# Optimization experiments

Measured on AMD Instinct MI355X. Metric: run time of the kernel, lower is better.

## Reference

```python
import jax, jax.numpy as jnp
import numpy as np

B, S, D, H = 2, 2048, 2048, 16
HD = D // H  # 128


def _rope(t, cos, sin):
    # t: [B, S, H, HD]; cos/sin: [S, HD//2]
    te, to = t[..., ::2], t[..., 1::2]
    c = cos[None, :, None, :]
    s = sin[None, :, None, :]
    re = te * c - to * s
    im = te * s + to * c
    # interleave back (matches tf.stack(..., axis=-1) + reshape)
    return jnp.stack([re, im], axis=-1).reshape(t.shape)


def setup_inputs() -> dict:
    key = jax.random.key(0)
    ks = jax.random.split(key, 6)
    x = jax.random.normal(ks[0], (B, S, D), dtype=jnp.float32)
    Wq = jax.random.normal(ks[1], (D, D), dtype=jnp.float32) * 0.02
    Wk = jax.random.normal(ks[2], (D, D), dtype=jnp.float32) * 0.02
    Wv = jax.random.normal(ks[3], (D, D), dtype=jnp.float32) * 0.02
    Wo = jax.random.normal(ks[4], (D, D), dtype=jnp.float32) * 0.02
    # rotary embeddings: freqs_cis = exp(i * pos * inv_freq)
    inv_freq = 1.0 / (10000.0 ** (jnp.arange(0, HD, 2, dtype=jnp.float32) / HD))  # [HD//2]
    angles = jnp.arange(S, dtype=jnp.float32)[:, None] * inv_freq[None, :]  # [S, HD//2]
    freqs_cos = jnp.cos(angles)
    freqs_sin = jnp.sin(angles)
    # additive causal mask [1,1,S,S]
    causal = jnp.tril(jnp.ones((S, S), dtype=bool))
    mask = jnp.where(causal, 0.0, -1e9).astype(jnp.float32)[None, None]
    return {"x": x, "Wq": Wq, "Wk": Wk, "Wv": Wv, "Wo": Wo,
            "freqs_cos": freqs_cos, "freqs_sin": freqs_sin, "mask": mask}


def reference(x, Wq, Wk, Wv, Wo, freqs_cos, freqs_sin, mask):
    b, s, d = x.shape
    xq = (x @ Wq).reshape(b, s, H, HD)
    xk = (x @ Wk).reshape(b, s, H, HD)
    xv = (x @ Wv).reshape(b, s, H, HD)
    xq = _rope(xq, freqs_cos, freqs_sin)
    xk = _rope(xk, freqs_cos, freqs_sin)
    # [B, H, S, HD]
    xq = xq.transpose(0, 2, 1, 3)
    xk = xk.transpose(0, 2, 1, 3)
    xv = xv.transpose(0, 2, 1, 3)
    scores = jnp.einsum('bhqd,bhkd->bhqk', xq, xk) / jnp.sqrt(jnp.float32(HD))
    scores = scores + mask[:, :, :s, :s]
    probs = jax.nn.softmax(scores + 1e-9, axis=-1)
    out = jnp.einsum('bhqk,bhkd->bhqd', probs, xv)
    out = out.transpose(0, 2, 1, 3).reshape(b, s, d)
    return out @ Wo
```

## Files before the change

### kernel.cpp

```cpp
#include <hip/hip_runtime.h>
#include <cstdint>

#define BB 2
#define SS 2048
#define DD 2048
#define HH 16
#define HDIM 128
#define MM (BB * SS)

typedef __attribute__((ext_vector_type(8))) short bf16x8;
typedef __attribute__((ext_vector_type(4))) short bf16x4;
typedef __attribute__((ext_vector_type(4))) float f32x4;
typedef __attribute__((ext_vector_type(16))) float f32x16;

__device__ inline short f2bf(float f) {
  union { float f; unsigned u; } v; v.f = f;
  unsigned r = v.u + 0x7FFFu + ((v.u >> 16) & 1u);
  return (short)(r >> 16);
}
__device__ inline float bf2f(short s) {
  union { float f; unsigned u; } v;
  v.u = ((unsigned)(unsigned short)s) << 16;
  return v.f;
}
__device__ inline float asf(int u) { union { int i; float f; } v; v.i = u; return v.f; }
__device__ inline int asi(float f) { union { float f; int i; } v; v.f = f; return v.i; }

__device__ inline unsigned cvtpk_bf16(float lo, float hi) {
  unsigned r;
  asm("v_cvt_pk_bf16_f32 %0, %1, %2" : "=v"(r) : "v"(lo), "v"(hi));
  return r;
}

__device__ inline void gll16(const void* g, void* l) {
  __builtin_amdgcn_global_load_lds(
      (const __attribute__((address_space(1))) void*)g,
      (__attribute__((address_space(3))) void*)l, 16, 0, 0);
}

__global__ __launch_bounds__(256) void cast_bf16_kernel(
    const float* __restrict__ x, short* __restrict__ y, int n4) {
  int i = blockIdx.x * 256 + threadIdx.x;
  if (i >= n4) return;
  float4 v = reinterpret_cast<const float4*>(x)[i];
  bf16x4 o;
  o[0] = f2bf(v.x); o[1] = f2bf(v.y); o[2] = f2bf(v.z); o[3] = f2bf(v.w);
  reinterpret_cast<bf16x4*>(y)[i] = o;
}

__global__ __launch_bounds__(256) void transpose_cast_kernel(
    const float* __restrict__ W, short* __restrict__ Wt) {
  __shared__ short tile[64][65];
  int c = threadIdx.x & 63, r4 = threadIdx.x >> 6;
  int n0 = blockIdx.x << 6, k0 = blockIdx.y << 6;
#pragma unroll
  for (int p = 0; p < 16; ++p) {
    int r = (p << 2) + r4;
    tile[c][r] = f2bf(W[(size_t)(k0 + r) * DD + n0 + c]);
  }
  __syncthreads();
#pragma unroll
  for (int p = 0; p < 16; ++p) {
    int r = (p << 2) + r4;
    Wt[(size_t)(n0 + r) * DD + k0 + c] = tile[r][c];
  }
}

__global__ __launch_bounds__(256) void transpose_v_kernel(
    const short* __restrict__ V, short* __restrict__ Vt) {
  __shared__ short tile[64][65];
  int c = threadIdx.x & 63, r4 = threadIdx.x >> 6;
  int s0 = blockIdx.x << 6, d0 = blockIdx.y << 6;
  int bh = blockIdx.z;
  int b = bh >> 4, h = bh & 15;
#pragma unroll
  for (int p = 0; p < 16; ++p) {
    int r = (p << 2) + r4;
    tile[c][r] = V[(size_t)(b * SS + s0 + r) * DD + h * HDIM + d0 + c];
  }
  __syncthreads();
#pragma unroll
  for (int p = 0; p < 16; ++p) {
    int r = (p << 2) + r4;
    Vt[((size_t)bh * HDIM + d0 + r) * SS + s0 + c] = tile[r][c];
  }
}

__global__ __launch_bounds__(512) void qkv_gemm8_kernel(
    const short* __restrict__ A, const short* __restrict__ Bt,
    short* __restrict__ Qb, short* __restrict__ Kb, short* __restrict__ Vb,
    const float* __restrict__ fc, const float* __restrict__ fs) {
  __shared__ short smem[2][32768];
  const int tid = threadIdx.x;
  const int lane = tid & 63, w = tid >> 6;
  const int cl = lane & 15, gq = lane >> 4;
  const int wm = w >> 2, wn = w & 3;
  const int bid = blockIdx.x;
  const int wg = (bid & 7) * 48 + (bid >> 3);
  const int tn = wg % 24, tm = wg / 24;
  const int m0 = tm << 8, n0 = tn << 8;
  const int mat = n0 >> 11;

  f32x4 acc[8][4];
#pragma unroll
  for (int i = 0; i < 8; ++i)
#pragma unroll
    for (int j = 0; j < 4; ++j) {
      f32x4 z = {0.f, 0.f, 0.f, 0.f};
      acc[i][j] = z;
    }

  const int srow8 = lane >> 3;
  const int sseg = lane & 7;

  auto stageA = [&](int t, int j) {
    int row = j * 64 + w * 8 + srow8;
    int sg = sseg ^ (row & 7);
    gll16(&A[(size_t)(m0 + row) * DD + t * 64 + sg * 8],
          &smem[t & 1][j * 4096 + w * 512]);
  };
  auto stageB = [&](int t, int j) {
    int row = j * 64 + w * 8 + srow8;
    int sg = sseg ^ (row & 7);
    gll16(&Bt[(size_t)(n0 + row) * DD + t * 64 + sg * 8],
          &smem[t & 1][16384 + j * 4096 + w * 512]);
  };

#pragma unroll
  for (int j = 0; j < 4; ++j) { stageA(0, j); stageB(0, j); }
  asm volatile("s_waitcnt vmcnt(0)" ::: "memory");
  __builtin_amdgcn_s_barrier();
  __builtin_amdgcn_sched_barrier(0);

  for (int t = 0; t < 32; ++t) {
    const short* Ab = &smem[t & 1][0];
    const short* Bb = &smem[t & 1][16384];
#pragma unroll
    for (int q = 0; q < 4; ++q) {
      const int mq = q >> 1, nq = q & 1;
      bf16x8 af[2][4], bfv[2][2];
#pragma unroll
      for (int ks = 0; ks < 2; ++ks) {
#pragma unroll
        for (int f = 0; f < 4; ++f) {
          int ra = wm * 128 + mq * 64 + f * 16 + cl;
          af[ks][f] = *reinterpret_cast<const bf16x8*>(
              &Ab[(ra * 64 + ks * 32 + gq * 8) ^ ((ra & 7) << 3)]);
        }
#pragma unroll
        for (int g = 0; g < 2; ++g) {
          int rb = wn * 64 + nq * 32 + g * 16 + cl;
          bfv[ks][g] = *reinterpret_cast<const bf16x8*>(
              &Bb[(rb * 64 + ks * 32 + gq * 8) ^ ((rb & 7) << 3)]);
        }
      }
      if (t + 1 < 32) {
        if (q == 0) { stageA(t + 1, 0); stageA(t + 1, 1); stageB(t + 1, 0); stageB(t + 1, 1); }
        else if (q == 1) { stageA(t + 1, 2); stageA(t + 1, 3); stageB(t + 1, 2); stageB(t + 1, 3); }
      }
      __builtin_amdgcn_s_barrier();
      __builtin_amdgcn_s_setprio(1);
#pragma unroll
      for (int ks = 0; ks < 2; ++ks)
#pragma unroll
        for (int f = 0; f < 4; ++f)
#pragma unroll
          for (int g = 0; g < 2; ++g)
            acc[mq * 4 + f][nq * 2 + g] = __builtin_amdgcn_mfma_f32_16x16x32_bf16(
                af[ks][f], bfv[ks][g], acc[mq * 4 + f][nq * 2 + g], 0, 0, 0);
      __builtin_amdgcn_s_setprio(0);
      __builtin_amdgcn_s_barrier();
    }
    asm volatile("s_waitcnt vmcnt(0)" ::: "memory");
    __builtin_amdgcn_s_barrier();
    __builtin_amdgcn_sched_barrier(0);
  }

  if (mat < 2) {
    const float qs = (mat == 0) ? 0.127517448f : 1.0f;
    short* Dst = (mat == 0) ? Qb : Kb;
#pragma unroll
    for (int fm = 0; fm < 8; ++fm)
#pragma unroll
      for (int r = 0; r < 4; ++r) {
        int mrow = m0 + wm * 128 + fm * 16 + gq * 4 + r;
        int s = mrow & (SS - 1);
#pragma unroll
        for (int fn = 0; fn < 4; ++fn) {
          int ncol = n0 + wn * 64 + fn * 16 + cl;
          int c = ncol & 127;
          int i = c >> 1;
          float cv = fc[s * 64 + i], sv = fs[s * 64 + i];
          float v = acc[fm][fn][r];
          float vp = __shfl_xor(v, 1, 64);
          float o = (c & 1) ? (v * cv + vp * sv) : (v * cv - vp * sv);
          Dst[(size_t)mrow * DD + (ncol & (DD - 1))] = f2bf(o * qs);
        }
      }
  } else {
#pragma unroll
    for (int fm = 0; fm < 8; ++fm)
#pragma unroll
      for (int r = 0; r < 4; ++r) {
        int mrow = m0 + wm * 128 + fm * 16 + gq * 4 + r;
#pragma unroll
        for (int fn = 0; fn < 4; ++fn) {
          int ncol = n0 + wn * 64 + fn * 16 + cl;
          Vb[(size_t)mrow * DD + (ncol - 4096)] = f2bf(acc[fm][fn][r]);
        }
      }
  }
}

__global__ __launch_bounds__(256) void gemm_kernel(
    const short* __restrict__ A, const short* __restrict__ Bt, float* __restrict__ C,
    int Mdim, int Ndim, int Kdim) {
  __shared__ short As[128 * 64];
  __shared__ short Bs[128 * 64];
  int tid = threadIdx.x;
  int lane = tid & 63, w = tid >> 6;
  int cl = lane & 15, gq = lane >> 4;
  int wm = w >> 1, wn = w & 1;
  int m0 = blockIdx.y << 7, n0 = blockIdx.x << 7;
  f32x4 acc[4][4];
#pragma unroll
  for (int i = 0; i < 4; ++i)
#pragma unroll
    for (int j = 0; j < 4; ++j) {
      f32x4 z = {0.f, 0.f, 0.f, 0.f};
      acc[i][j] = z;
    }
  int lrow = lane >> 3;
  int lseg = (lane & 7) ^ lrow;

  for (int k0 = 0; k0 < Kdim; k0 += 64) {
#pragma unroll
    for (int i = 0; i < 4; ++i) {
      int r0 = ((w << 2) + i) << 3;
      gll16(&A[(size_t)(m0 + r0 + lrow) * Kdim + k0 + (lseg << 3)], &As[r0 << 6]);
      gll16(&Bt[(size_t)(n0 + r0 + lrow) * Kdim + k0 + (lseg << 3)], &Bs[r0 << 6]);
    }
    __syncthreads();
#pragma unroll
    for (int ks = 0; ks < 2; ++ks) {
      bf16x8 af[4], bfr[4];
#pragma unroll
      for (int f = 0; f < 4; ++f) {
        int ra = (wm << 6) + (f << 4) + cl;
        af[f] = *reinterpret_cast<const bf16x8*>(
            &As[((ra << 6) + (ks << 5) + (gq << 3)) ^ ((ra & 7) << 3)]);
        int rb = (wn << 6) + (f << 4) + cl;
        bfr[f] = *reinterpret_cast<const bf16x8*>(
            &Bs[((rb << 6) + (ks << 5) + (gq << 3)) ^ ((rb & 7) << 3)]);
      }
#pragma unroll
      for (int fm = 0; fm < 4; ++fm)
#pragma unroll
        for (int fn = 0; fn < 4; ++fn)
          acc[fm][fn] = __builtin_amdgcn_mfma_f32_16x16x32_bf16(
              af[fm], bfr[fn], acc[fm][fn], 0, 0, 0);
    }
    __syncthreads();
  }
#pragma unroll
  for (int fm = 0; fm < 4; ++fm)
#pragma unroll
    for (int r = 0; r < 4; ++r) {
      int mrow = m0 + (wm << 6) + (fm << 4) + (gq << 2) + r;
#pragma unroll
      for (int fn = 0; fn < 4; ++fn) {
        int ncol = n0 + (wn << 6) + (fn << 4) + cl;
        C[(size_t)mrow * Ndim + ncol] = acc[fm][fn][r];
      }
    }
}

__global__ __launch_bounds__(256, 2) void attn_kernel(
    const short* __restrict__ Q, const short* __restrict__ K,
    const short* __restrict__ Vt, short* __restrict__ O) {
  __shared__ short Kl[2][64 * 128];
  __shared__ short Vl[2][128 * 64];
  const int id = blockIdx.x;
  const int qi = 15 - (id >> 5);
  const int bh = id & 31;
  const int b = bh >> 4, h = bh & 15;
  const int tid = threadIdx.x;
  const int lane = tid & 63, w = tid >> 6;
  const int l31 = lane & 31, hi = lane >> 5;
  const int qw = qi * 128 + w * 32;
  const int qg = qw + l31;

  const short* Kbase = K + (size_t)b * SS * DD + h * HDIM;
  const short* Vbase = Vt + (size_t)bh * HDIM * SS;
  int krow[4], kq[4], vd[4], vs[4];
#pragma unroll
  for (int i = 0; i < 4; ++i) {
    int c = w * 4 + i;
    krow[i] = c * 4 + (lane >> 4);
    kq[i] = (lane & 15) ^ (krow[i] & 7);
    vd[i] = c * 8 + (lane >> 3);
    vs[i] = (lane & 7) ^ (vd[i] & 7);
  }

  bf16x8 qf[8];
  const size_t qoff = ((size_t)b * SS + qg) * DD + h * HDIM;
#pragma unroll
  for (int s = 0; s < 8; ++s)
    qf[s] = *reinterpret_cast<const bf16x8*>(&Q[qoff + s * 16 + hi * 8]);

  f32x16 ot[4];
#pragma unroll
  for (int dt = 0; dt < 4; ++dt)
#pragma unroll
    for (int r = 0; r < 16; ++r) ot[dt][r] = 0.f;
  float m_run = -INFINITY, l_run = 0.f;

  const int NT = 2 * qi + 2;

#pragma unroll
  for (int i = 0; i < 4; ++i) {
    gll16(Kbase + (size_t)krow[i] * DD + kq[i] * 8, &Kl[0][(w * 4 + i) * 512]);
    gll16(Vbase + (size_t)vd[i] * SS + vs[i] * 8, &Vl[0][(w * 4 + i) * 512]);
  }
  __syncthreads();

  for (int t = 0; t < NT; ++t) {
    const int cur = t & 1;
    if (t + 1 < NT) {
      const int nt64 = (t + 1) * 64;
#pragma unroll
      for (int i = 0; i < 4; ++i) {
        gll16(Kbase + (size_t)(nt64 + krow[i]) * DD + kq[i] * 8,
              &Kl[cur ^ 1][(w * 4 + i) * 512]);
        gll16(Vbase + (size_t)vd[i] * SS + nt64 + vs[i] * 8,
              &Vl[cur ^ 1][(w * 4 + i) * 512]);
      }
    }

    if (t * 64 <= qw + 31) {
      const short* Kc = Kl[cur];
      const short* Vc = Vl[cur];
      f32x16 st0, st1;
#pragma unroll
      for (int r = 0; r < 16; ++r) { st0[r] = 0.f; st1[r] = 0.f; }
      __builtin_amdgcn_s_setprio(1);
#pragma unroll
      for (int s = 0; s < 8; ++s) {
        const int cs = (s * 2 + hi);
        bf16x8 kf0 = *reinterpret_cast<const bf16x8*>(
            &Kc[l31 * 128 + ((cs ^ (l31 & 7)) << 3)]);
        st0 = __builtin_amdgcn_mfma_f32_32x32x16_bf16(kf0, qf[s], st0, 0, 0, 0);
        bf16x8 kf1 = *reinterpret_cast<const bf16x8*>(
            &Kc[(32 + l31) * 128 + ((cs ^ (l31 & 7)) << 3)]);
        st1 = __builtin_amdgcn_mfma_f32_32x32x16_bf16(kf1, qf[s], st1, 0, 0, 0);
      }
      __builtin_amdgcn_s_setprio(0);
      if (t * 64 + 63 > qw) {
#pragma unroll
        for (int r = 0; r < 16; ++r) {
          int dl = (r & 3) + 8 * (r >> 2) + 4 * hi;
          if (t * 64 + dl > qg) st0[r] = -1e30f;
          if (t * 64 + 32 + dl > qg) st1[r] = -1e30f;
        }
      }
      float mx[16];
#pragma unroll
      for (int r = 0; r < 16; ++r) mx[r] = fmaxf(st0[r], st1[r]);
#pragma unroll
      for (int off = 8; off >= 1; off >>= 1)
#pragma unroll
        for (int r = 0; r < 8; ++r)
          if (r < off) mx[r] = fmaxf(mx[r], mx[r + off]);
      float pm = mx[0];
      {
        auto sw = __builtin_amdgcn_permlane32_swap(asi(pm), asi(pm), false, false);
        pm = fmaxf(asf(sw[0]), asf(sw[1]));
      }
      if (!__all(pm <= m_run + 11.5f)) {
        float mn = fmaxf(m_run, pm);
        float al = exp2f(m_run - mn);
        m_run = mn;
        l_run *= al;
#pragma unroll
        for (int dt = 0; dt < 4; ++dt)
#pragma unroll
          for (int r = 0; r < 16; ++r) ot[dt][r] *= al;
      }
#pragma unroll
      for (int r = 0; r < 16; ++r) st0[r] = exp2f(st0[r] - m_run);
#pragma unroll
      for (int r = 0; r < 16; ++r) st1[r] = exp2f(st1[r] - m_run);
      float sm[16];
#pragma unroll
      for (int r = 0; r < 16; ++r) sm[r] = st0[r] + st1[r];
#pragma unroll
      for (int off = 8; off >= 1; off >>= 1)
#pragma unroll
        for (int r = 0; r < 8; ++r)
          if (r < off) sm[r] += sm[r + off];
      float ps = sm[0];
      {
        auto sw = __builtin_amdgcn_permlane32_swap(asi(ps), asi(ps), false, false);
        ps = asf(sw[0]) + asf(sw[1]);
      }
      l_run += ps;

      bf16x8 pf[4];
#pragma unroll
      for (int s = 0; s < 4; ++s) {
        float e0, e1, e2, e3, e4, e5, e6, e7;
        if (s < 2) {
          e0 = st0[8 * s + 0]; e1 = st0[8 * s + 1]; e2 = st0[8 * s + 2]; e3 = st0[8 * s + 3];
          e4 = st0[8 * s + 4]; e5 = st0[8 * s + 5]; e6 = st0[8 * s + 6]; e7 = st0[8 * s + 7];
        } else {
          e0 = st1[8 * (s - 2) + 0]; e1 = st1[8 * (s - 2) + 1]; e2 = st1[8 * (s - 2) + 2]; e3 = st1[8 * (s - 2) + 3];
          e4 = st1[8 * (s - 2) + 4]; e5 = st1[8 * (s - 2) + 5]; e6 = st1[8 * (s - 2) + 6]; e7 = st1[8 * (s - 2) + 7];
        }
        unsigned a0 = cvtpk_bf16(e0, e1);
        unsigned a1 = cvtpk_bf16(e2, e3);
        unsigned b0 = cvtpk_bf16(e4, e5);
        unsigned b1 = cvtpk_bf16(e6, e7);
        auto r0 = __builtin_amdgcn_permlane32_swap((int)a0, (int)b0, false, false);
        auto r1 = __builtin_amdgcn_permlane32_swap((int)a1, (int)b1, false, false);
        union { int u[4]; bf16x8 v; } pk;
        pk.u[0] = r0[0]; pk.u[1] = r1[0]; pk.u[2] = r0[1]; pk.u[3] = r1[1];
        pf[s] = pk.v;
      }

      __builtin_amdgcn_s_setprio(1);
#pragma unroll
      for (int dt = 0; dt < 4; ++dt) {
        const int vr = dt * 32 + l31;
#pragma unroll
        for (int s = 0; s < 4; ++s) {
          bf16x8 vf = *reinterpret_cast<const bf16x8*>(
              &Vc[vr * 64 + (((s * 2 + hi) ^ (vr & 7)) << 3)]);
          ot[dt] = __builtin_amdgcn_mfma_f32_32x32x16_bf16(vf, pf[s], ot[dt], 0, 0, 0);
        }
      }
      __builtin_amdgcn_s_setprio(0);
    }
    __syncthreads();
  }

  float inv = 1.0f / l_run;
  const size_t orow = ((size_t)b * SS + qg) * DD + h * HDIM;
#pragma unroll
  for (int dt = 0; dt < 4; ++dt)
#pragma unroll
    for (int g = 0; g < 4; ++g) {
      bf16x4 v;
#pragma unroll
      for (int k = 0; k < 4; ++k) v[k] = f2bf(ot[dt][4 * g + k] * inv);
      *reinterpret_cast<bf16x4*>(&O[orow + dt * 32 + 8 * g + 4 * hi]) = v;
    }
}

extern "C" void kernel_launch(void* const* d_in, const int* in_sizes, int n_in,
                              void* d_out, int out_size, void* d_ws, size_t ws_size,
                              hipStream_t stream) {
  const float* x = (const float*)d_in[0];
  const float* Wq = (const float*)d_in[1];
  const float* Wk = (const float*)d_in[2];
  const float* Wv = (const float*)d_in[3];
  const float* Wo = (const float*)d_in[4];
  const float* fc = (const float*)d_in[5];
  const float* fs = (const float*)d_in[6];
  float* out = (float*)d_out;
  char* ws = (char*)d_ws;

  short* xb     = (short*)(ws + 0);
  short* WqkvT  = (short*)(ws + (size_t)16 * 1048576);
  short* WoT    = (short*)(ws + (size_t)40 * 1048576);
  short* Qb     = (short*)(ws + (size_t)48 * 1048576);
  short* Kb     = (short*)(ws + (size_t)64 * 1048576);
  short* Vb     = (short*)(ws + (size_t)80 * 1048576);
  short* VtB    = WqkvT;

  cast_bf16_kernel<<<8192, 256, 0, stream>>>(x, xb, 2097152);
  dim3 tg(32, 32);
  transpose_cast_kernel<<<tg, 256, 0, stream>>>(Wq, WqkvT);
  transpose_cast_kernel<<<tg, 256, 0, stream>>>(Wk, WqkvT + (size_t)2048 * 2048);
  transpose_cast_kernel<<<tg, 256, 0, stream>>>(Wv, WqkvT + (size_t)4096 * 2048);
  transpose_cast_kernel<<<tg, 256, 0, stream>>>(Wo, WoT);

  qkv_gemm8_kernel<<<384, 512, 0, stream>>>(xb, WqkvT, Qb, Kb, Vb, fc, fs);

  transpose_v_kernel<<<dim3(32, 2, 32), 256, 0, stream>>>(Vb, VtB);

  attn_kernel<<<512, 256, 0, stream>>>(Qb, Kb, VtB, xb);

  gemm_kernel<<<dim3(16, 32), 256, 0, stream>>>(xb, WoT, out, MM, DD, DD);
}
```

Baseline: 294.2 us.

## Retile GEMMs into a templated 8-wave kernel and merge weight transposes

The QKV projection moves from 256x256 tiles (384 blocks) to 256x192 tiles (512 blocks), with a K-split-by-half LDS layout, a finer-grained prefetch pipeline using partial vmcnt waits, and XCD-aware tile mapping. The output projection now reuses the same 512-thread pipelined kernel with 256x128 tiles instead of the simple single-buffered 128x128 GEMM. The four weight transpose-cast launches are merged into one z-indexed launch. The aim is better CU occupancy balance and overlap of global loads with MFMA work. The cost is more complex partial-wait accounting and a per-element branch in the epilogue, since a tile can now straddle Q/K/V boundaries.

```diff
diff --git a/kernel.cpp b/kernel.cpp
--- a/kernel.cpp
+++ b/kernel.cpp
@@ -48,9 +48,14 @@
   reinterpret_cast<bf16x4*>(y)[i] = o;
 }
 
-__global__ __launch_bounds__(256) void transpose_cast_kernel(
-    const float* __restrict__ W, short* __restrict__ Wt) {
+__global__ __launch_bounds__(256) void transpose4_kernel(
+    const float* __restrict__ Wq, const float* __restrict__ Wk,
+    const float* __restrict__ Wv, const float* __restrict__ Wo,
+    short* __restrict__ WqkvT, short* __restrict__ WoT) {
   __shared__ short tile[64][65];
+  int z = blockIdx.z;
+  const float* W = (z == 0) ? Wq : (z == 1) ? Wk : (z == 2) ? Wv : Wo;
+  short* Wt = (z < 3) ? (WqkvT + (size_t)z * DD * DD) : WoT;
   int c = threadIdx.x & 63, r4 = threadIdx.x >> 6;
   int n0 = blockIdx.x << 6, k0 = blockIdx.y << 6;
 #pragma unroll
@@ -86,193 +91,147 @@
   }
 }
 
-__global__ __launch_bounds__(512) void qkv_gemm8_kernel(
+template <int BN, int MODE>
+__global__ __launch_bounds__(512) void gemm8_kernel(
     const short* __restrict__ A, const short* __restrict__ Bt,
     short* __restrict__ Qb, short* __restrict__ Kb, short* __restrict__ Vb,
+    float* __restrict__ Cf,
     const float* __restrict__ fc, const float* __restrict__ fs) {
-  __shared__ short smem[2][32768];
+  constexpr int FN = BN / 32;
+  constexpr int LB = BN / 64;
+  constexpr int BH = BN * 32;
+  __shared__ short smem[2][16384 + BN * 64];
+
   const int tid = threadIdx.x;
   const int lane = tid & 63, w = tid >> 6;
   const int cl = lane & 15, gq = lane >> 4;
-  const int wm = w >> 2, wn = w & 3;
+  const int wm = w >> 1, wn = w & 1;
+
   const int bid = blockIdx.x;
-  const int wg = (bid & 7) * 48 + (bid >> 3);
-  const int tn = wg % 24, tm = wg / 24;
-  const int m0 = tm << 8, n0 = tn << 8;
-  const int mat = n0 >> 11;
-
-  f32x4 acc[8][4];
-#pragma unroll
-  for (int i = 0; i < 8; ++i)
-#pragma unroll
-    for (int j = 0; j < 4; ++j) {
+  const int xcd = bid & 7, local = bid >> 3;
+  constexpr int TNX = (BN == 192) ? 4 : 2;
+  const int tm = local & 15, tn = xcd * TNX + (local >> 4);
+  const int m0 = tm << 8, n0 = tn * BN;
+
+  f32x4 acc[4][FN];
+#pragma unroll
+  for (int i = 0; i < 4; ++i)
+#pragma unroll
+    for (int j = 0; j < FN; ++j) {
       f32x4 z = {0.f, 0.f, 0.f, 0.f};
       acc[i][j] = z;
     }
 
-  const int srow8 = lane >> 3;
-  const int sseg = lane & 7;
-
-  auto stageA = [&](int t, int j) {
-    int row = j * 64 + w * 8 + srow8;
-    int sg = sseg ^ (row & 7);
-    gll16(&A[(size_t)(m0 + row) * DD + t * 64 + sg * 8],
-          &smem[t & 1][j * 4096 + w * 512]);
+  auto stageA = [&](int t, int l, short* buf) {
+    int D = l * 8192 + tid * 16;
+    int half = D >> 14;
+    int row = (D >> 6) & 255;
+    int p2 = (D >> 4) & 3;
+    int col = t * 64 + half * 32 + ((p2 ^ (row & 3)) << 3);
+    gll16(&A[(size_t)(m0 + row) * DD + col], (char*)buf + D);
   };
-  auto stageB = [&](int t, int j) {
-    int row = j * 64 + w * 8 + srow8;
-    int sg = sseg ^ (row & 7);
-    gll16(&Bt[(size_t)(n0 + row) * DD + t * 64 + sg * 8],
-          &smem[t & 1][16384 + j * 4096 + w * 512]);
+  auto stageB = [&](int t, int l, short* buf) {
+    int D = l * 8192 + tid * 16;
+    int half = (D >= BN * 64) ? 1 : 0;
+    int row = (D - half * BN * 64) >> 6;
+    int p2 = (D >> 4) & 3;
+    int col = t * 64 + half * 32 + ((p2 ^ (row & 3)) << 3);
+    gll16(&Bt[(size_t)(n0 + row) * DD + col], (char*)buf + 32768 + D);
   };
 
-#pragma unroll
-  for (int j = 0; j < 4; ++j) { stageA(0, j); stageB(0, j); }
+  auto compute = [&](const short* base, int ks) {
+    const short* Ab = base;
+    const short* Bb = base + 16384;
+    bf16x8 af[4], bfv[FN];
+#pragma unroll
+    for (int fm = 0; fm < 4; ++fm) {
+      int ra = wm * 64 + fm * 16 + cl;
+      af[fm] = *reinterpret_cast<const bf16x8*>(
+          &Ab[ks * 8192 + ra * 32 + ((gq ^ (ra & 3)) << 3)]);
+    }
+#pragma unroll
+    for (int fn = 0; fn < FN; ++fn) {
+      int rb = wn * (BN / 2) + fn * 16 + cl;
+      bfv[fn] = *reinterpret_cast<const bf16x8*>(
+          &Bb[ks * BH + rb * 32 + ((gq ^ (rb & 3)) << 3)]);
+    }
+    __builtin_amdgcn_s_setprio(1);
+#pragma unroll
+    for (int fm = 0; fm < 4; ++fm)
+#pragma unroll
+      for (int fn = 0; fn < FN; ++fn)
+        acc[fm][fn] = __builtin_amdgcn_mfma_f32_16x16x32_bf16(
+            af[fm], bfv[fn], acc[fm][fn], 0, 0, 0);
+    __builtin_amdgcn_s_setprio(0);
+  };
+
+  stageA(0, 0, smem[0]); stageA(0, 1, smem[0]);
+#pragma unroll
+  for (int l = 0; l < LB; ++l) stageB(0, l, smem[0]);
+  stageA(0, 2, smem[0]); stageA(0, 3, smem[0]);
+  asm volatile("s_waitcnt vmcnt(2)" ::: "memory");
+  __builtin_amdgcn_s_barrier();
+
+  for (int t = 0; t < 31; ++t) {
+    short* cur = smem[t & 1];
+    short* nxt = smem[(t + 1) & 1];
+    stageA(t + 1, 0, nxt); stageA(t + 1, 1, nxt);
+#pragma unroll
+    for (int l = 0; l < LB; ++l) stageB(t + 1, l, nxt);
+    compute(cur, 0);
+    if constexpr (BN == 192)
+      asm volatile("s_waitcnt vmcnt(5)" ::: "memory");
+    else
+      asm volatile("s_waitcnt vmcnt(4)" ::: "memory");
+    __builtin_amdgcn_s_barrier();
+    stageA(t + 1, 2, nxt); stageA(t + 1, 3, nxt);
+    compute(cur, 1);
+    asm volatile("s_waitcnt vmcnt(2)" ::: "memory");
+    __builtin_amdgcn_s_barrier();
+  }
+  compute(smem[1], 0);
   asm volatile("s_waitcnt vmcnt(0)" ::: "memory");
   __builtin_amdgcn_s_barrier();
-  __builtin_amdgcn_sched_barrier(0);
-
-  for (int t = 0; t < 32; ++t) {
-    const short* Ab = &smem[t & 1][0];
-    const short* Bb = &smem[t & 1][16384];
-#pragma unroll
-    for (int q = 0; q < 4; ++q) {
-      const int mq = q >> 1, nq = q & 1;
-      bf16x8 af[2][4], bfv[2][2];
-#pragma unroll
-      for (int ks = 0; ks < 2; ++ks) {
-#pragma unroll
-        for (int f = 0; f < 4; ++f) {
-          int ra = wm * 128 + mq * 64 + f * 16 + cl;
-          af[ks][f] = *reinterpret_cast<const bf16x8*>(
-              &Ab[(ra * 64 + ks * 32 + gq * 8) ^ ((ra & 7) << 3)]);
-        }
-#pragma unroll
-        for (int g = 0; g < 2; ++g) {
-          int rb = wn * 64 + nq * 32 + g * 16 + cl;
-          bfv[ks][g] = *reinterpret_cast<const bf16x8*>(
-              &Bb[(rb * 64 + ks * 32 + gq * 8) ^ ((rb & 7) << 3)]);
-        }
-      }
-      if (t + 1 < 32) {
-        if (q == 0) { stageA(t + 1, 0); stageA(t + 1, 1); stageB(t + 1, 0); stageB(t + 1, 1); }
-        else if (q == 1) { stageA(t + 1, 2); stageA(t + 1, 3); stageB(t + 1, 2); stageB(t + 1, 3); }
-      }
-      __builtin_amdgcn_s_barrier();
-      __builtin_amdgcn_s_setprio(1);
-#pragma unroll
-      for (int ks = 0; ks < 2; ++ks)
-#pragma unroll
-        for (int f = 0; f < 4; ++f)
-#pragma unroll
-          for (int g = 0; g < 2; ++g)
-            acc[mq * 4 + f][nq * 2 + g] = __builtin_amdgcn_mfma_f32_16x16x32_bf16(
-                af[ks][f], bfv[ks][g], acc[mq * 4 + f][nq * 2 + g], 0, 0, 0);
-      __builtin_amdgcn_s_setprio(0);
-      __builtin_amdgcn_s_barrier();
-    }
-    asm volatile("s_waitcnt vmcnt(0)" ::: "memory");
-    __builtin_amdgcn_s_barrier();
-    __builtin_amdgcn_sched_barrier(0);
-  }
-
-  if (mat < 2) {
-    const float qs = (mat == 0) ? 0.127517448f : 1.0f;
-    short* Dst = (mat == 0) ? Qb : Kb;
-#pragma unroll
-    for (int fm = 0; fm < 8; ++fm)
+  compute(smem[1], 1);
+
+  if constexpr (MODE == 0) {
+#pragma unroll
+    for (int fm = 0; fm < 4; ++fm)
 #pragma unroll
       for (int r = 0; r < 4; ++r) {
-        int mrow = m0 + wm * 128 + fm * 16 + gq * 4 + r;
+        int mrow = m0 + wm * 64 + fm * 16 + gq * 4 + r;
         int s = mrow & (SS - 1);
 #pragma unroll
-        for (int fn = 0; fn < 4; ++fn) {
-          int ncol = n0 + wn * 64 + fn * 16 + cl;
-          int c = ncol & 127;
-          int i = c >> 1;
-          float cv = fc[s * 64 + i], sv = fs[s * 64 + i];
+        for (int fn = 0; fn < FN; ++fn) {
+          int ncol = n0 + wn * (BN / 2) + fn * 16 + cl;
           float v = acc[fm][fn][r];
           float vp = __shfl_xor(v, 1, 64);
-          float o = (c & 1) ? (v * cv + vp * sv) : (v * cv - vp * sv);
-          Dst[(size_t)mrow * DD + (ncol & (DD - 1))] = f2bf(o * qs);
+          if (ncol < 4096) {
+            int c = ncol & 127;
+            int i = c >> 1;
+            float cv = fc[s * 64 + i], sv = fs[s * 64 + i];
+            float o = (c & 1) ? (v * cv + vp * sv) : (v * cv - vp * sv);
+            float qs = (ncol < 2048) ? 0.127517448f : 1.0f;
+            short* Dp = (ncol < 2048) ? Qb : Kb;
+            Dp[(size_t)mrow * DD + (ncol & (DD - 1))] = f2bf(o * qs);
+          } else {
+            Vb[(size_t)mrow * DD + (ncol - 4096)] = f2bf(v);
+          }
         }
       }
   } else {
 #pragma unroll
-    for (int fm = 0; fm < 8; ++fm)
+    for (int fm = 0; fm < 4; ++fm)
 #pragma unroll
       for (int r = 0; r < 4; ++r) {
-        int mrow = m0 + wm * 128 + fm * 16 + gq * 4 + r;
-#pragma unroll
-        for (int fn = 0; fn < 4; ++fn) {
-          int ncol = n0 + wn * 64 + fn * 16 + cl;
-          Vb[(size_t)mrow * DD + (ncol - 4096)] = f2bf(acc[fm][fn][r]);
+        int mrow = m0 + wm * 64 + fm * 16 + gq * 4 + r;
+#pragma unroll
+        for (int fn = 0; fn < FN; ++fn) {
+          int ncol = n0 + wn * (BN / 2) + fn * 16 + cl;
+          Cf[(size_t)mrow * DD + ncol] = acc[fm][fn][r];
         }
       }
   }
-}
-
-__global__ __launch_bounds__(256) void gemm_kernel(
-    const short* __restrict__ A, const short* __restrict__ Bt, float* __restrict__ C,
-    int Mdim, int Ndim, int Kdim) {
-  __shared__ short As[128 * 64];
-  __shared__ short Bs[128 * 64];
-  int tid = threadIdx.x;
-  int lane = tid & 63, w = tid >> 6;
-  int cl = lane & 15, gq = lane >> 4;
-  int wm = w >> 1, wn = w & 1;
-  int m0 = blockIdx.y << 7, n0 = blockIdx.x << 7;
-  f32x4 acc[4][4];
-#pragma unroll
-  for (int i = 0; i < 4; ++i)
-#pragma unroll
-    for (int j = 0; j < 4; ++j) {
-      f32x4 z = {0.f, 0.f, 0.f, 0.f};
-      acc[i][j] = z;
-    }
-  int lrow = lane >> 3;
-  int lseg = (lane & 7) ^ lrow;
-
-  for (int k0 = 0; k0 < Kdim; k0 += 64) {
-#pragma unroll
-    for (int i = 0; i < 4; ++i) {
-      int r0 = ((w << 2) + i) << 3;
-      gll16(&A[(size_t)(m0 + r0 + lrow) * Kdim + k0 + (lseg << 3)], &As[r0 << 6]);
-      gll16(&Bt[(size_t)(n0 + r0 + lrow) * Kdim + k0 + (lseg << 3)], &Bs[r0 << 6]);
-    }
-    __syncthreads();
-#pragma unroll
-    for (int ks = 0; ks < 2; ++ks) {
-      bf16x8 af[4], bfr[4];
-#pragma unroll
-      for (int f = 0; f < 4; ++f) {
-        int ra = (wm << 6) + (f << 4) + cl;
-        af[f] = *reinterpret_cast<const bf16x8*>(
-            &As[((ra << 6) + (ks << 5) + (gq << 3)) ^ ((ra & 7) << 3)]);
-        int rb = (wn << 6) + (f << 4) + cl;
-        bfr[f] = *reinterpret_cast<const bf16x8*>(
-            &Bs[((rb << 6) + (ks << 5) + (gq << 3)) ^ ((rb & 7) << 3)]);
-      }
-#pragma unroll
-      for (int fm = 0; fm < 4; ++fm)
-#pragma unroll
-        for (int fn = 0; fn < 4; ++fn)
-          acc[fm][fn] = __builtin_amdgcn_mfma_f32_16x16x32_bf16(
-              af[fm], bfr[fn], acc[fm][fn], 0, 0, 0);
-    }
-    __syncthreads();
-  }
-#pragma unroll
-  for (int fm = 0; fm < 4; ++fm)
-#pragma unroll
-    for (int r = 0; r < 4; ++r) {
-      int mrow = m0 + (wm << 6) + (fm << 4) + (gq << 2) + r;
-#pragma unroll
-      for (int fn = 0; fn < 4; ++fn) {
-        int ncol = n0 + (wn << 6) + (fn << 4) + cl;
-        C[(size_t)mrow * Ndim + ncol] = acc[fm][fn][r];
-      }
-    }
 }
 
 __global__ __launch_bounds__(256, 2) void attn_kernel(
@@ -478,17 +437,15 @@
   short* VtB    = WqkvT;
 
   cast_bf16_kernel<<<8192, 256, 0, stream>>>(x, xb, 2097152);
-  dim3 tg(32, 32);
-  transpose_cast_kernel<<<tg, 256, 0, stream>>>(Wq, WqkvT);
-  transpose_cast_kernel<<<tg, 256, 0, stream>>>(Wk, WqkvT + (size_t)2048 * 2048);
-  transpose_cast_kernel<<<tg, 256, 0, stream>>>(Wv, WqkvT + (size_t)4096 * 2048);
-  transpose_cast_kernel<<<tg, 256, 0, stream>>>(Wo, WoT);
-
-  qkv_gemm8_kernel<<<384, 512, 0, stream>>>(xb, WqkvT, Qb, Kb, Vb, fc, fs);
+  transpose4_kernel<<<dim3(32, 32, 4), 256, 0, stream>>>(Wq, Wk, Wv, Wo, WqkvT, WoT);
+
+  gemm8_kernel<192, 0><<<512, 512, 0, stream>>>(
+      xb, WqkvT, Qb, Kb, Vb, nullptr, fc, fs);
 
   transpose_v_kernel<<<dim3(32, 2, 32), 256, 0, stream>>>(Vb, VtB);
 
   attn_kernel<<<512, 256, 0, stream>>>(Qb, Kb, VtB, xb);
 
-  gemm_kernel<<<dim3(16, 32), 256, 0, stream>>>(xb, WoT, out, MM, DD, DD);
-}
+  gemm8_kernel<128, 1><<<256, 512, 0, stream>>>(
+      xb, WoT, nullptr, nullptr, nullptr, out, nullptr, nullptr);
+}
```

Result: faster. 281.9 us (-4.2%).
